# Optimization experiments

Hardware: AMD Instinct MI355X
Metric: run time of the kernel (lower is better)

The kernel has to match this reference:

```python
import jax, jax.numpy as jnp
import numpy as np

# FlowNetC correlation config (matches init_kwargs)
PAD = 20          # pad_size
KERNEL = 1        # kernel_size (kernel_radius = 0)
MAX_DISP = 20     # max_displacement
STRIDE1 = 1       # output stride
STRIDE2 = 2       # displacement stride
RAD = MAX_DISP // STRIDE2   # neighborhood_grid_radius = 10 -> 21x21 = 441 displacements


def setup_inputs() -> dict:
    key = jax.random.key(0)
    k1, k2 = jax.random.split(key)
    B, C, H, W = 4, 256, 64, 96
    return {
        "input1": jax.random.normal(k1, (B, C, H, W), dtype=jnp.float32),
        "input2": jax.random.normal(k2, (B, C, H, W), dtype=jnp.float32),
    }


def reference(input1, input2):
    # input1, input2: [B, C, H, W]
    # Output: [B, (2*RAD+1)**2, H, W]  (pad_size == max_displacement, stride1 == 1,
    # kernel_size == 1 => output spatial size equals input spatial size).
    B, C, H, W = input1.shape
    p2 = jnp.pad(input2, ((0, 0), (0, 0), (PAD, PAD), (PAD, PAD)))
    norm = jnp.asarray(KERNEL * KERNEL * C, dtype=input1.dtype)
    outs = []
    # Fixed, small displacement grid (21x21): static slicing per displacement
    # avoids materializing a [441, B, C, H, W] intermediate.
    for dy in range(-RAD, RAD + 1):
        oy = PAD + dy * STRIDE2
        for dx in range(-RAD, RAD + 1):
            ox = PAD + dx * STRIDE2
            shifted = p2[:, :, oy:oy + H, ox:ox + W]        # [B, C, H, W]
            outs.append(jnp.sum(input1 * shifted, axis=1))  # [B, H, W]
    corr = jnp.stack(outs, axis=1) / norm                    # [B, 441, H, W]
    return corr
```

## Files before the change

kernel.cpp:

```cpp
#include <hip/hip_runtime.h>


typedef short bf16x8 __attribute__((ext_vector_type(8)));
typedef float f32x4  __attribute__((ext_vector_type(4)));

#define PLANE 24576
#define ST    40

__device__ __forceinline__ short f2bf(float f) {
    union { float f; unsigned u; } x; x.f = f;
    const unsigned u = x.u;
    return (short)((u + 0x7fffu + ((u >> 16) & 1u)) >> 16);
}

__global__ __launch_bounds__(512)
void corr_prepass(const float* __restrict__ in1, const float* __restrict__ in2,
                  short* __restrict__ dstA, short* __restrict__ dstB) {
    const int bid = blockIdx.x;
    const int sel = bid >> 8;
    const int r   = bid & 255;
    const int b   = r >> 6;
    const int yt  = (r >> 3) & 7;
    const int ct  = r & 7;
    const int c0 = ct * 32, y0 = yt * 8;
    const float* src = sel ? in2 : in1;
    short* dst = sel ? dstB : dstA;

    __shared__ __align__(16) short T[768 * ST];
    const int tid = threadIdx.x;

#pragma unroll
    for (int it = 0; it < 2; ++it) {
        const int d = it * 512 + tid;
        if (d < 768) {
            const int g = d / 192;
            const int f = d - g * 192;
            float4 v[8];
#pragma unroll
            for (int j = 0; j < 8; ++j) {
                const int c = c0 + g * 8 + j;
                v[j] = *(const float4*)(src + ((size_t)(b * 256 + c) * 64 + y0) * 96 + 4 * f);
            }
            bf16x8 w0, w1, w2, w3;
#pragma unroll
            for (int j = 0; j < 8; ++j) {
                w0[j] = f2bf(v[j].x); w1[j] = f2bf(v[j].y);
                w2[j] = f2bf(v[j].z); w3[j] = f2bf(v[j].w);
            }
            const int perm = ((g ^ (f & 3)) * 8);
            const int base = 4 * f * ST + perm;
            *(bf16x8*)&T[base]          = w0;
            *(bf16x8*)&T[base + ST]     = w1;
            *(bf16x8*)&T[base + 2*ST]   = w2;
            *(bf16x8*)&T[base + 3*ST]   = w3;
        }
    }
    __syncthreads();

#pragma unroll
    for (int it = 0; it < 6; ++it) {
        const int D  = it * 512 + tid;
        const int Rl = D >> 2, gp = D & 3;
        const int yy  = Rl / 96;
        const int rl  = Rl - yy * 96;
        const int par = rl / 48;
        const int col = rl - par * 48;
        const int x   = 2 * col + par;
        const int xx  = yy * 96 + x;
        const int perm = ((gp ^ ((xx >> 2) & 3)) * 8);
        const bf16x8 w = *(const bf16x8*)&T[xx * ST + perm];
        const size_t Rg = (size_t)(b * 64 + y0 + yy) * 96 + par * 48 + col;
        *(bf16x8*)(dst + Rg * 256 + c0 + gp * 8) = w;
    }
}

#define GLOAD(dst, ptr, imm) \
    asm volatile("global_load_dwordx4 %0, %1, off offset:%c2" \
                 : "=&v"(dst) : "v"(ptr), "n"(imm) : "memory")
#define WAITV0 \
    asm volatile("s_waitcnt vmcnt(0)"); \
    __builtin_amdgcn_sched_barrier(0)

#define MFMA16(A, B, C) __builtin_amdgcn_mfma_f32_16x16x32_bf16(A, B, C, 0, 0, 0)

__global__ __launch_bounds__(384, 3)
void corr_mfma(const short* __restrict__ Ag, const short* __restrict__ Bg,
               float* __restrict__ out) {
    const int bhw = blockIdx.x;
    const int bid = ((bhw & 7) << 6) | (bhw >> 3);
    const int xcd = bid >> 6;
    const int b   = xcd >> 1;
    const int zhi = xcd & 1;
    const int inner = bid & 63;
    const int par = inner & 1;
    const int z   = (zhi << 5) | (inner >> 1);

    const int tid  = threadIdx.x;
    const int lane = tid & 63, slot = tid >> 6;
    const int n    = lane & 15, q = lane >> 4;

    __shared__ __align__(16) short Bsh[2][48 * 256];
    __shared__ __align__(16) float scr[6][528];

    const int y2o = (z < 62) ? (z + 2) : (z - 62);

    {
        const short* se = Bg + (size_t)(b * 64 + z)   * PLANE + par * 48 * 256;
        const short* so = Bg + (size_t)(b * 64 + y2o) * PLANE + par * 48 * 256;
#pragma unroll
        for (int it = 0; it < 4; ++it) {
            const int j   = it * 384 + tid;
            const int row = j >> 5;
            const int ofs = (row * 256 + (j & 31) * 8) ^ ((row & 7) << 3);
            *(bf16x8*)&Bsh[0][ofs] = *(const bf16x8*)(se + j * 8);
        }
#pragma unroll
        for (int it = 0; it < 4; ++it) {
            const int j   = it * 384 + tid;
            const int row = j >> 5;
            const int ofs = (row * 256 + (j & 31) * 8) ^ ((row & 7) << 3);
            *(bf16x8*)&Bsh[1][ofs] = *(const bf16x8*)(so + j * 8);
        }
    }
    __syncthreads();

    const bool v0 = (n >= 10), v3 = (n < 10);
    const int r0 = v0 ? (n - 10) : 0;
    const int r1 = n + 6;
    const int r2 = n + 22;
    const int r3 = v3 ? (n + 38) : 0;
    float* const sc = scr[slot];

#define STEPX(ks, ab, BS, AC) { \
    const int ko = (ks) * 32 + q * 8; \
    bf16x8 b0 = *(const bf16x8*)&BS[(r0 * 256 + ko) ^ ((r0 & 7) << 3)]; if (!v0) b0 = 0; \
    bf16x8 b1 = *(const bf16x8*)&BS[(r1 * 256 + ko) ^ ((r1 & 7) << 3)]; \
    bf16x8 b2 = *(const bf16x8*)&BS[(r2 * 256 + ko) ^ ((r2 & 7) << 3)]; \
    bf16x8 b3 = *(const bf16x8*)&BS[(r3 * 256 + ko) ^ ((r3 & 7) << 3)]; if (!v3) b3 = 0; \
    AC[0] = MFMA16(ab[0], b0, AC[0]); \
    AC[1] = MFMA16(ab[0], b1, AC[1]); \
    AC[2] = MFMA16(ab[0], b2, AC[2]); \
    AC[3] = MFMA16(ab[1], b1, AC[3]); \
    AC[4] = MFMA16(ab[1], b2, AC[4]); \
    AC[5] = MFMA16(ab[1], b3, AC[5]); \
    AC[6] = MFMA16(ab[2], b2, AC[6]); \
    AC[7] = MFMA16(ab[2], b3, AC[7]); }

#define GL12(P0, P1, P2, BASE) \
    GLOAD(a0[0], P0, (BASE) + 0);   GLOAD(a0[1], P1, (BASE) + 0);   GLOAD(a0[2], P2, (BASE) + 0);   \
    GLOAD(a1[0], P0, (BASE) + 64);  GLOAD(a1[1], P1, (BASE) + 64);  GLOAD(a1[2], P2, (BASE) + 64);  \
    GLOAD(a2[0], P0, (BASE) + 128); GLOAD(a2[1], P1, (BASE) + 128); GLOAD(a2[2], P2, (BASE) + 128); \
    GLOAD(a3[0], P0, (BASE) + 192); GLOAD(a3[1], P1, (BASE) + 192); GLOAD(a3[2], P2, (BASE) + 192);

#define EPILOG(DYP, Y, AC) { \
    const int mb = q * 4; \
    _Pragma("unroll") \
    for (int kp = 0; kp < 2; ++kp) { \
        const int k0 = kp ? 11 : 0; \
        const int kn = kp ? 10 : 11; \
        _Pragma("unroll") \
        for (int t2 = 0; t2 < 9; ++t2) { \
            const int Xi = (t2 < 3) ? 0 : (t2 < 6 ? 1 : 2); \
            constexpr int UJ[9] = {0, 1, 2, 1, 2, 3, 2, 3, 4}; \
            const int ub = UJ[t2] * 16; \
            _Pragma("unroll") \
            for (int rr = 0; rr < 4; ++rr) { \
                const int xe = Xi * 16 + mb + rr; \
                const int k  = ub + n - xe; \
                if ((unsigned)(k - k0) < (unsigned)kn) \
                    sc[xe * 11 + (k - k0)] = AC[t2][rr]; \
            } \
        } \
        const size_t ob = ((size_t)(b * 441 + (DYP) * 21 + k0) * 64 + (Y)) * 96 + par; \
        const int nit = kp ? 8 : 9; \
        _Pragma("unroll") \
        for (int it2 = 0; it2 < 9; ++it2) { \
            if (it2 < nit) { \
                const int e = it2 * 64 + lane; \
                if (e < kn * 48) { \
                    const int k  = e / 48; \
                    const int xe = e - k * 48; \
                    out[ob + (size_t)k * 6144 + 2 * xe] = sc[xe * 11 + k] * (1.0f / 256.0f); \
                } \
            } \
        } \
    } }

#pragma unroll
    for (int p = 0; p < 2; ++p) {
        const int m = p * 6 + slot;
        if (m >= 11) continue;
        const int dyp_e = 2 * m, dyp_o = 2 * m + 1;
        const int y_e = z   + 20 - 4 * m;
        const int y_o = y2o + 18 - 4 * m;
        const bool live_e = (y_e >= 0) && (y_e < 64);
        const bool live_o = (m < 10) && (y_o >= 0) && (y_o < 64);
        if (!live_e && !live_o) continue;

        const int  y_ld = live_e ? y_e : y_o;
        const bool rld  = live_o && (y_o != y_ld);

        const short* ApL = Ag + ((size_t)(b * 64 + y_ld) * 96 + par * 48) * 256
                         + n * 256 + q * 8;
        const short* l0 = ApL, *l1 = ApL + 4096, *l2 = ApL + 8192;
        const short* ApO = Ag + ((size_t)(b * 64 + y_o) * 96 + par * 48) * 256
                         + n * 256 + q * 8;
        const short* o0 = ApO, *o1 = ApO + 4096, *o2 = ApO + 8192;

        f32x4 accE[9], accO[9];
#pragma unroll
        for (int t = 0; t < 9; ++t) { accE[t] = (f32x4)0.0f; accO[t] = (f32x4)0.0f; }

        bf16x8 a0[3], a1[3], a2[3], a3[3];

        GL12(l0, l1, l2, 0) WAITV0;
        if (live_e) {
            STEPX(0, a0, Bsh[0], accE) STEPX(1, a1, Bsh[0], accE)
            STEPX(2, a2, Bsh[0], accE) STEPX(3, a3, Bsh[0], accE)
        }
        if (live_o) {
            if (rld) { GL12(o0, o1, o2, 0) WAITV0; }
            STEPX(0, a0, Bsh[1], accO) STEPX(1, a1, Bsh[1], accO)
            STEPX(2, a2, Bsh[1], accO) STEPX(3, a3, Bsh[1], accO)
        }
        GL12(l0, l1, l2, 256) WAITV0;
        if (live_e) {
            STEPX(4, a0, Bsh[0], accE) STEPX(5, a1, Bsh[0], accE)
            STEPX(6, a2, Bsh[0], accE) STEPX(7, a3, Bsh[0], accE)
        }
        if (live_o) {
            if (rld) { GL12(o0, o1, o2, 256) WAITV0; }
            STEPX(4, a0, Bsh[1], accO) STEPX(5, a1, Bsh[1], accO)
            STEPX(6, a2, Bsh[1], accO) STEPX(7, a3, Bsh[1], accO)
        }

        if (live_e) EPILOG(dyp_e, y_e, accE)
        if (live_o) EPILOG(dyp_o, y_o, accO)
    }
#undef STEPX
#undef GL12
#undef EPILOG
}

extern "C" void kernel_launch(void* const* d_in, const int* in_sizes, int n_in,
                              void* d_out, int out_size, void* d_ws, size_t ws_size,
                              hipStream_t stream) {
    const float* in1 = (const float*)d_in[0];
    const float* in2 = (const float*)d_in[1];
    float* out = (float*)d_out;

    short* Ag = (short*)d_ws;
    short* Bg = Ag + (size_t)256 * PLANE;

    corr_prepass<<<dim3(512), dim3(512), 0, stream>>>(in1, in2, Ag, Bg);
    corr_mfma<<<dim3(512), dim3(384), 0, stream>>>(Ag, Bg, out);
}
```

Before: 144.7 us.

## Widen MFMA correlation blocks to eight waves and software-pipeline A-operand loads

Raises the correlation kernel from 6 to 8 waves per block, with 2 blocks per CU instead of 3, and resizes the shared-memory scratch and the B-tile staging loops to match. The inline-asm global loads and their full vmcnt waits are replaced by plain loads. A single A fetch now feeds both the even and odd displacement accumulators, and the next K-slice of A is prefetched while the current one's MFMAs run, so fewer waits land on the critical path. In exchange, both accumulator sets are always computed even when one output row is out of range, and the 11 row-groups now split 8+3 across waves, which leaves some waves idle in the second pass.

```diff
diff --git a/kernel.cpp b/kernel.cpp
--- a/kernel.cpp
+++ b/kernel.cpp
@@ -74,16 +74,9 @@
     }
 }
 
-#define GLOAD(dst, ptr, imm) \
-    asm volatile("global_load_dwordx4 %0, %1, off offset:%c2" \
-                 : "=&v"(dst) : "v"(ptr), "n"(imm) : "memory")
-#define WAITV0 \
-    asm volatile("s_waitcnt vmcnt(0)"); \
-    __builtin_amdgcn_sched_barrier(0)
-
 #define MFMA16(A, B, C) __builtin_amdgcn_mfma_f32_16x16x32_bf16(A, B, C, 0, 0, 0)
 
-__global__ __launch_bounds__(384, 3)
+__global__ __launch_bounds__(512, 2)
 void corr_mfma(const short* __restrict__ Ag, const short* __restrict__ Bg,
                float* __restrict__ out) {
     const int bhw = blockIdx.x;
@@ -100,7 +93,7 @@
     const int n    = lane & 15, q = lane >> 4;
 
     __shared__ __align__(16) short Bsh[2][48 * 256];
-    __shared__ __align__(16) float scr[6][528];
+    __shared__ __align__(16) float scr[8][528];
 
     const int y2o = (z < 62) ? (z + 2) : (z - 62);
 
@@ -108,15 +101,15 @@
         const short* se = Bg + (size_t)(b * 64 + z)   * PLANE + par * 48 * 256;
         const short* so = Bg + (size_t)(b * 64 + y2o) * PLANE + par * 48 * 256;
 #pragma unroll
-        for (int it = 0; it < 4; ++it) {
-            const int j   = it * 384 + tid;
+        for (int it = 0; it < 3; ++it) {
+            const int j   = it * 512 + tid;
             const int row = j >> 5;
             const int ofs = (row * 256 + (j & 31) * 8) ^ ((row & 7) << 3);
             *(bf16x8*)&Bsh[0][ofs] = *(const bf16x8*)(se + j * 8);
         }
 #pragma unroll
-        for (int it = 0; it < 4; ++it) {
-            const int j   = it * 384 + tid;
+        for (int it = 0; it < 3; ++it) {
+            const int j   = it * 512 + tid;
             const int row = j >> 5;
             const int ofs = (row * 256 + (j & 31) * 8) ^ ((row & 7) << 3);
             *(bf16x8*)&Bsh[1][ofs] = *(const bf16x8*)(so + j * 8);
@@ -131,26 +124,39 @@
     const int r3 = v3 ? (n + 38) : 0;
     float* const sc = scr[slot];
 
-#define STEPX(ks, ab, BS, AC) { \
+#define LOADA(buf, ks) \
+    buf[0] = *(const bf16x8*)(Ap + 0 * 4096 + (ks) * 32); \
+    buf[1] = *(const bf16x8*)(Ap + 1 * 4096 + (ks) * 32); \
+    buf[2] = *(const bf16x8*)(Ap + 2 * 4096 + (ks) * 32);
+
+#define DSTEP(ks, ab, PF) { \
     const int ko = (ks) * 32 + q * 8; \
-    bf16x8 b0 = *(const bf16x8*)&BS[(r0 * 256 + ko) ^ ((r0 & 7) << 3)]; if (!v0) b0 = 0; \
-    bf16x8 b1 = *(const bf16x8*)&BS[(r1 * 256 + ko) ^ ((r1 & 7) << 3)]; \
-    bf16x8 b2 = *(const bf16x8*)&BS[(r2 * 256 + ko) ^ ((r2 & 7) << 3)]; \
-    bf16x8 b3 = *(const bf16x8*)&BS[(r3 * 256 + ko) ^ ((r3 & 7) << 3)]; if (!v3) b3 = 0; \
-    AC[0] = MFMA16(ab[0], b0, AC[0]); \
-    AC[1] = MFMA16(ab[0], b1, AC[1]); \
-    AC[2] = MFMA16(ab[0], b2, AC[2]); \
-    AC[3] = MFMA16(ab[1], b1, AC[3]); \
-    AC[4] = MFMA16(ab[1], b2, AC[4]); \
-    AC[5] = MFMA16(ab[1], b3, AC[5]); \
-    AC[6] = MFMA16(ab[2], b2, AC[6]); \
-    AC[7] = MFMA16(ab[2], b3, AC[7]); }
-
-#define GL12(P0, P1, P2, BASE) \
-    GLOAD(a0[0], P0, (BASE) + 0);   GLOAD(a0[1], P1, (BASE) + 0);   GLOAD(a0[2], P2, (BASE) + 0);   \
-    GLOAD(a1[0], P0, (BASE) + 64);  GLOAD(a1[1], P1, (BASE) + 64);  GLOAD(a1[2], P2, (BASE) + 64);  \
-    GLOAD(a2[0], P0, (BASE) + 128); GLOAD(a2[1], P1, (BASE) + 128); GLOAD(a2[2], P2, (BASE) + 128); \
-    GLOAD(a3[0], P0, (BASE) + 192); GLOAD(a3[1], P1, (BASE) + 192); GLOAD(a3[2], P2, (BASE) + 192);
+    bf16x8 e0 = *(const bf16x8*)&Bsh[0][(r0 * 256 + ko) ^ ((r0 & 7) << 3)]; if (!v0) e0 = 0; \
+    bf16x8 e1 = *(const bf16x8*)&Bsh[0][(r1 * 256 + ko) ^ ((r1 & 7) << 3)]; \
+    bf16x8 e2 = *(const bf16x8*)&Bsh[0][(r2 * 256 + ko) ^ ((r2 & 7) << 3)]; \
+    bf16x8 e3 = *(const bf16x8*)&Bsh[0][(r3 * 256 + ko) ^ ((r3 & 7) << 3)]; if (!v3) e3 = 0; \
+    accE[0] = MFMA16(ab[0], e0, accE[0]); \
+    accE[1] = MFMA16(ab[0], e1, accE[1]); \
+    accE[2] = MFMA16(ab[0], e2, accE[2]); \
+    accE[3] = MFMA16(ab[1], e1, accE[3]); \
+    accE[4] = MFMA16(ab[1], e2, accE[4]); \
+    accE[5] = MFMA16(ab[1], e3, accE[5]); \
+    accE[6] = MFMA16(ab[2], e2, accE[6]); \
+    accE[7] = MFMA16(ab[2], e3, accE[7]); \
+    bf16x8 o0 = *(const bf16x8*)&Bsh[1][(r0 * 256 + ko) ^ ((r0 & 7) << 3)]; if (!v0) o0 = 0; \
+    bf16x8 o1 = *(const bf16x8*)&Bsh[1][(r1 * 256 + ko) ^ ((r1 & 7) << 3)]; \
+    bf16x8 o2 = *(const bf16x8*)&Bsh[1][(r2 * 256 + ko) ^ ((r2 & 7) << 3)]; \
+    bf16x8 o3 = *(const bf16x8*)&Bsh[1][(r3 * 256 + ko) ^ ((r3 & 7) << 3)]; if (!v3) o3 = 0; \
+    accO[0] = MFMA16(ab[0], o0, accO[0]); \
+    accO[1] = MFMA16(ab[0], o1, accO[1]); \
+    accO[2] = MFMA16(ab[0], o2, accO[2]); \
+    accO[3] = MFMA16(ab[1], o1, accO[3]); \
+    accO[4] = MFMA16(ab[1], o2, accO[4]); \
+    accO[5] = MFMA16(ab[1], o3, accO[5]); \
+    accO[6] = MFMA16(ab[2], o2, accO[6]); \
+    accO[7] = MFMA16(ab[2], o3, accO[7]); \
+    if (PF) { LOADA(ab, (ks) + 4) } \
+}
 
 #define EPILOG(DYP, Y, AC) { \
     const int mb = q * 4; \
@@ -188,7 +194,7 @@
 
 #pragma unroll
     for (int p = 0; p < 2; ++p) {
-        const int m = p * 6 + slot;
+        const int m = p * 8 + slot;
         if (m >= 11) continue;
         const int dyp_e = 2 * m, dyp_o = 2 * m + 1;
         const int y_e = z   + 20 - 4 * m;
@@ -197,48 +203,25 @@
         const bool live_o = (m < 10) && (y_o >= 0) && (y_o < 64);
         if (!live_e && !live_o) continue;
 
-        const int  y_ld = live_e ? y_e : y_o;
-        const bool rld  = live_o && (y_o != y_ld);
-
-        const short* ApL = Ag + ((size_t)(b * 64 + y_ld) * 96 + par * 48) * 256
-                         + n * 256 + q * 8;
-        const short* l0 = ApL, *l1 = ApL + 4096, *l2 = ApL + 8192;
-        const short* ApO = Ag + ((size_t)(b * 64 + y_o) * 96 + par * 48) * 256
-                         + n * 256 + q * 8;
-        const short* o0 = ApO, *o1 = ApO + 4096, *o2 = ApO + 8192;
+        const int y_ld = live_e ? y_e : y_o;
+        const short* Ap = Ag + ((size_t)(b * 64 + y_ld) * 96 + par * 48) * 256
+                        + n * 256 + q * 8;
 
         f32x4 accE[9], accO[9];
 #pragma unroll
         for (int t = 0; t < 9; ++t) { accE[t] = (f32x4)0.0f; accO[t] = (f32x4)0.0f; }
 
         bf16x8 a0[3], a1[3], a2[3], a3[3];
-
-        GL12(l0, l1, l2, 0) WAITV0;
-        if (live_e) {
-            STEPX(0, a0, Bsh[0], accE) STEPX(1, a1, Bsh[0], accE)
-            STEPX(2, a2, Bsh[0], accE) STEPX(3, a3, Bsh[0], accE)
-        }
-        if (live_o) {
-            if (rld) { GL12(o0, o1, o2, 0) WAITV0; }
-            STEPX(0, a0, Bsh[1], accO) STEPX(1, a1, Bsh[1], accO)
-            STEPX(2, a2, Bsh[1], accO) STEPX(3, a3, Bsh[1], accO)
-        }
-        GL12(l0, l1, l2, 256) WAITV0;
-        if (live_e) {
-            STEPX(4, a0, Bsh[0], accE) STEPX(5, a1, Bsh[0], accE)
-            STEPX(6, a2, Bsh[0], accE) STEPX(7, a3, Bsh[0], accE)
-        }
-        if (live_o) {
-            if (rld) { GL12(o0, o1, o2, 256) WAITV0; }
-            STEPX(4, a0, Bsh[1], accO) STEPX(5, a1, Bsh[1], accO)
-            STEPX(6, a2, Bsh[1], accO) STEPX(7, a3, Bsh[1], accO)
-        }
+        LOADA(a0, 0) LOADA(a1, 1) LOADA(a2, 2) LOADA(a3, 3)
+
+        DSTEP(0, a0, 1) DSTEP(1, a1, 1) DSTEP(2, a2, 1) DSTEP(3, a3, 1)
+        DSTEP(4, a0, 0) DSTEP(5, a1, 0) DSTEP(6, a2, 0) DSTEP(7, a3, 0)
 
         if (live_e) EPILOG(dyp_e, y_e, accE)
         if (live_o) EPILOG(dyp_o, y_o, accO)
     }
-#undef STEPX
-#undef GL12
+#undef DSTEP
+#undef LOADA
 #undef EPILOG
 }
 
@@ -253,5 +236,5 @@
     short* Bg = Ag + (size_t)256 * PLANE;
 
     corr_prepass<<<dim3(512), dim3(512), 0, stream>>>(in1, in2, Ag, Bg);
-    corr_mfma<<<dim3(512), dim3(384), 0, stream>>>(Ag, Bg, out);
-}
+    corr_mfma<<<dim3(512), dim3(512), 0, stream>>>(Ag, Bg, out);
+}
```

After: 133.6 us, median of 2. 1.08x faster.
